# Optimization experiments

Hardware: AMD Instinct MI355X
Metric: run time of the kernel (lower is better)

Reference implementation:

```python
import jax, jax.numpy as jnp
import numpy as np

B, IN, OUT = 2048, 64, 2048


def setup_inputs() -> dict:
    key = jax.random.key(0)
    k1, k2, k3 = jax.random.split(key, 3)
    x = jax.random.normal(k1, (B, IN), dtype=jnp.float32)
    # learned params (shapes per init: means [in, out], inv_std_dev [out, in, in])
    means = jax.random.uniform(k2, (IN, OUT), dtype=jnp.float32)
    # roughly like the inverse of a diagonal step matrix plus small noise
    inv_std_dev = (jax.random.normal(k3, (OUT, IN, IN), dtype=jnp.float32) * 0.05
                   + jnp.eye(IN, dtype=jnp.float32) * 0.5)
    return {"x": x, "means": means, "inv_std_dev": inv_std_dev}


def reference(x, means, inv_std_dev):
    # diff[b, o, i] = x[b, i] - means[i, o]   -> [B, OUT, IN]
    d = x[:, None, :] - means.T[None, :, :]
    # torch uses inv_std_dev.pow(2) (elementwise square), not a matrix square
    A = inv_std_dev * inv_std_dev  # [OUT, IN, IN]
    # per-neuron quadratic form: q[b, o] = d[b,o,:] @ A[o] @ d[b,o,:]
    q = jnp.einsum('boi,oij,boj->bo', d, A, d)
    return jnp.exp(-0.5 * q)  # [B, OUT]
```

## Files before the change

### kernel.cpp

```cpp
#include <hip/hip_runtime.h>
#include <hip/hip_bf16.h>

typedef __bf16 bf16x8 __attribute__((ext_vector_type(8)));
typedef float f32x4 __attribute__((ext_vector_type(4)));
typedef float f32x16 __attribute__((ext_vector_type(16)));

#define B_N 2048
#define O_N 2048
#define K_TRI 2080
#define K_TOT 2304
#define K_STEPS 36
#define STEP_B 131072

__device__ __forceinline__ void gld16(const void* g, void* l) {
    __builtin_amdgcn_global_load_lds(
        (const __attribute__((address_space(1))) void*)g,
        (__attribute__((address_space(3))) void*)l,
        16, 0, 0);
}

__global__ __launch_bounds__(256) void rbf_prepA(
    const float* __restrict__ inv, const float* __restrict__ means,
    const float* __restrict__ x, __bf16* __restrict__ Srm,
    __bf16* __restrict__ Pt)
{
    __shared__ float s[64 * 65];
    __shared__ float mld[64];
    __shared__ float uw[128];
    __shared__ unsigned short ptab[K_TRI];

    const int t = threadIdx.x;
    {
        int base = 0;
#pragma unroll 1
        for (int i = 0; i < 64; ++i) {
            if (t < 64 - i) ptab[base + t] = (unsigned short)((i << 8) | (i + t));
            base += 64 - i;
        }
    }

    if ((int)blockIdx.x < O_N) {
        const int o = blockIdx.x;
        const float4* src = (const float4*)(inv + (size_t)o * 4096);
#pragma unroll
        for (int k = 0; k < 4; ++k) {
            const int idx = k * 256 + t;
            const float4 v = src[idx];
            const int i = idx >> 4;
            const int j0 = (idx & 15) * 4;
            s[i * 65 + j0 + 0] = v.x * v.x;
            s[i * 65 + j0 + 1] = v.y * v.y;
            s[i * 65 + j0 + 2] = v.z * v.z;
            s[i * 65 + j0 + 3] = v.w * v.w;
        }
        if (t < 64) mld[t] = means[(size_t)t * O_N + o];
        __syncthreads();
        if (t < 64) {
            float u = 0.f;
#pragma unroll
            for (int i = 0; i < 64; ++i) u = fmaf(s[i * 65 + t], mld[i], u);
            uw[t] = u;
        } else if (t < 128) {
            const int j = t - 64;
            float w = 0.f;
#pragma unroll
            for (int i = 0; i < 64; ++i) w = fmaf(s[j * 65 + i], mld[i], w);
            uw[64 + j] = w;
        }
        __syncthreads();
        __bf16* Srow = Srm + (size_t)o * K_TOT;
#pragma unroll 1
        for (int c = t; c < K_TOT; c += 256) {
            float v;
            if (c < K_TRI) {
                const int ij = ptab[c];
                const int i = ij >> 8, j = ij & 255;
                v = (i == j) ? s[i * 65 + i] : (s[i * 65 + j] + s[j * 65 + i]);
            } else if (c < 2272) {
                const int j = (c - K_TRI) & 63;
                const float cv = -(uw[j] + uw[64 + j]);
                const __bf16 hi = (__bf16)cv;
                v = (c < 2208) ? (float)hi : (cv - (float)hi);
            } else if (c < 2274) {
                float kk = 0.f;
#pragma unroll
                for (int j = 0; j < 64; ++j) kk = fmaf(uw[j], mld[j], kk);
                const __bf16 khi = (__bf16)kk;
                v = (c == 2272) ? (float)khi : (kk - (float)khi);
            } else v = 0.f;
            Srow[c] = (__bf16)v;
        }
    } else {
        const int b0r = ((int)blockIdx.x - O_N) * 8;
#pragma unroll
        for (int q = 0; q < 2; ++q) {
            const int idx = q * 256 + t;
            s[(idx >> 6) * 65 + (idx & 63)] =
                x[(size_t)(b0r + (idx >> 6)) * 64 + (idx & 63)];
        }
        __syncthreads();
#pragma unroll 1
        for (int q = 0; q < 9; ++q) {
            const int task = q * 256 + t;
            const int c8 = task >> 3, r8 = task & 7;
            const float* xr = &s[r8 * 65];
            unsigned short w8[8];
#pragma unroll
            for (int e = 0; e < 8; ++e) {
                const int c = c8 * 8 + e;
                float v;
                if (c < K_TRI) {
                    const int ij = ptab[c];
                    v = xr[ij >> 8] * xr[ij & 255];
                } else if (c < 2272) {
                    const float xv = xr[(c - K_TRI) & 63];
                    const __bf16 hi = (__bf16)xv;
                    v = (c < 2144) ? (float)hi
                      : (c < 2208) ? (xv - (float)hi) : (float)hi;
                } else if (c < 2274) v = 1.f;
                else v = 0.f;
                w8[e] = __builtin_bit_cast(unsigned short, (__bf16)v);
            }
            *(bf16x8*)(Pt + ((size_t)c8 * 2048 + b0r + r8) * 8) =
                *(const bf16x8*)w8;
        }
    }
}

__global__ __launch_bounds__(256, 2) void rbf_prepB(
    const __bf16* __restrict__ Srm, __bf16* __restrict__ St)
{
    __shared__ __align__(16) char ts[64 * 1156];
    const int t = threadIdx.x;
    const int tb = (int)blockIdx.x >> 2;
    const int cp = (int)blockIdx.x & 3;
    const int o0 = tb * 64;

#pragma unroll 1
    for (int q = 0; q < 18; ++q) {
        const int idx = q * 256 + t;
        const int r = idx / 72, c = idx % 72;
        const float4 v = *(const float4*)((const char*)Srm
                          + (size_t)(o0 + r) * (K_TOT * 2) + cp * 1152 + c * 16);
        *(float4*)(&ts[r * 1156 + c * 16]) = v;
    }
    __syncthreads();
#pragma unroll 1
    for (int q = 0; q < 18; ++q) {
        const int idx = q * 256 + t;
        const int c = idx >> 6, r = idx & 63;
        const float4 v = *(const float4*)(&ts[r * 1156 + c * 16]);
        *(float4*)((char*)St + ((size_t)(cp * 72 + c) * 2048 + o0 + r) * 16) = v;
    }
}

__global__ __launch_bounds__(256, 2) void rbf_gemm_sk(
    const __bf16* __restrict__ P, const __bf16* __restrict__ S,
    float* __restrict__ Cpart)
{
    __shared__ __align__(16) char sAB[4][16384];

    const int tid = threadIdx.x;
    const int lane = tid & 63;
    const int w = tid >> 6;
    const int wr = w >> 1, wc = w & 1;
    const int cl = lane & 31;
    const int h = lane >> 5;

    const int wg = (int)blockIdx.x;
    const int xcd = wg & 7;
    const int loc = wg >> 3;
    const int kh = loc & 1;
    const int opan = (loc >> 1) & 1;
    const int bpan = loc >> 2;
    const int oBase = (xcd * 2 + opan) * 128;
    const int bBase = bpan * 128;
    const int kc = kh * 144;

    const char* gsrc[4];
#pragma unroll
    for (int q = 0; q < 4; ++q) {
        const int ks = (q & 1) * 2 + (tid >> 7);
        const int row = tid & 127;
        gsrc[q] = (q < 2)
            ? (const char*)P + ((size_t)(kc + ks) * 2048 + bBase + row) * 16
            : (const char*)S + ((size_t)(kc + ks) * 2048 + oBase + row) * 16;
    }

#define RBF_STAGE(ST) do {                                                    \
    const size_t go_ = (size_t)(ST) * STEP_B;                                 \
    char* d_ = &sAB[(ST) & 3][0];                                             \
    gld16(gsrc[0] + go_, d_ + 0    + tid * 16);                               \
    gld16(gsrc[1] + go_, d_ + 4096 + tid * 16);                               \
    gld16(gsrc[2] + go_, d_ + 8192  + tid * 16);                              \
    gld16(gsrc[3] + go_, d_ + 12288 + tid * 16);                              \
} while (0)

    RBF_STAGE(0);
    RBF_STAGE(1);

    const f32x16 zz = {0.f,0.f,0.f,0.f,0.f,0.f,0.f,0.f,
                       0.f,0.f,0.f,0.f,0.f,0.f,0.f,0.f};
    f32x16 acc00 = zz, acc01 = zz, acc10 = zz, acc11 = zz;

    const int aoff = (wr * 64 + cl) * 16;
    const int boff = 8192 + (wc * 64 + cl) * 16;

#pragma unroll 1
    for (int st = 0; st < K_STEPS; ++st) {
        if (st + 2 < K_STEPS) {
            RBF_STAGE(st + 2);
            asm volatile("s_waitcnt vmcnt(8)" ::: "memory");
        } else if (st + 1 < K_STEPS) {
            asm volatile("s_waitcnt vmcnt(4)" ::: "memory");
        } else {
            asm volatile("s_waitcnt vmcnt(0)" ::: "memory");
        }
        __builtin_amdgcn_s_barrier();
        __builtin_amdgcn_sched_barrier(0);
        const char* bp = &sAB[st & 3][0];

        __builtin_amdgcn_s_setprio(1);
#pragma unroll
        for (int s = 0; s < 2; ++s) {
            const int kso = (s * 2 + h) * 2048;
            const bf16x8 a0 = *(const bf16x8*)(bp + kso + aoff);
            const bf16x8 a1 = *(const bf16x8*)(bp + kso + aoff + 512);
            const bf16x8 b0 = *(const bf16x8*)(bp + kso + boff);
            const bf16x8 b1 = *(const bf16x8*)(bp + kso + boff + 512);
            acc00 = __builtin_amdgcn_mfma_f32_32x32x16_bf16(a0, b0, acc00, 0, 0, 0);
            acc01 = __builtin_amdgcn_mfma_f32_32x32x16_bf16(a0, b1, acc01, 0, 0, 0);
            acc10 = __builtin_amdgcn_mfma_f32_32x32x16_bf16(a1, b0, acc10, 0, 0, 0);
            acc11 = __builtin_amdgcn_mfma_f32_32x32x16_bf16(a1, b1, acc11, 0, 0, 0);
        }
        __builtin_amdgcn_s_setprio(0);
    }
#undef RBF_STAGE

    float* Cp = Cpart + (size_t)kh * O_N * B_N;
#pragma unroll
    for (int r = 0; r < 16; ++r) {
        const int row32 = (r & 3) + 8 * (r >> 2) + 4 * h;
        const size_t r0 = (size_t)(bBase + wr * 64 + row32) * O_N;
        const size_t r1 = (size_t)(bBase + wr * 64 + 32 + row32) * O_N;
        const int c0 = oBase + wc * 64 + cl;
        const int c1 = oBase + wc * 64 + 32 + cl;
        Cp[r0 + c0] = acc00[r];
        Cp[r0 + c1] = acc01[r];
        Cp[r1 + c0] = acc10[r];
        Cp[r1 + c1] = acc11[r];
    }
}

__global__ __launch_bounds__(256) void rbf_reduce(
    const float* __restrict__ C0, const float* __restrict__ C1,
    float* __restrict__ out)
{
    const size_t base = ((size_t)blockIdx.x * 256 + threadIdx.x) * 8;
#pragma unroll
    for (int q = 0; q < 2; ++q) {
        const size_t i = base + q * 4;
        const f32x4 a = *(const f32x4*)(C0 + i);
        const f32x4 b = *(const f32x4*)(C1 + i);
        f32x4 r;
#pragma unroll
        for (int e = 0; e < 4; ++e)
            r[e] = exp2f((a[e] + b[e]) * -0.72134752044448170368f);
        *(f32x4*)(out + i) = r;
    }
}

extern "C" void kernel_launch(void* const* d_in, const int* in_sizes, int n_in,
                              void* d_out, int out_size, void* d_ws, size_t ws_size,
                              hipStream_t stream)
{
    const float* x = (const float*)d_in[0];
    const float* means = (const float*)d_in[1];
    const float* inv = (const float*)d_in[2];
    float* out = (float*)d_out;

    const size_t SZ = (size_t)O_N * K_TOT * sizeof(__bf16);
    const size_t CZ = (size_t)O_N * B_N * sizeof(float);
    __bf16* St  = (__bf16*)d_ws;
    __bf16* Pt  = (__bf16*)((char*)d_ws + SZ);
    __bf16* Srm = (__bf16*)((char*)d_ws + 2 * SZ);
    float*  C0  = (float*)((char*)d_ws + 3 * SZ);
    float*  C1  = (float*)((char*)d_ws + 3 * SZ + CZ);

    rbf_prepA<<<dim3(O_N + 256), dim3(256), 0, stream>>>(inv, means, x, Srm, Pt);
    rbf_prepB<<<dim3(128), dim3(256), 0, stream>>>(Srm, St);
    rbf_gemm_sk<<<dim3(512), dim3(256), 0, stream>>>(Pt, St, C0);
    rbf_reduce<<<dim3(2048), dim3(256), 0, stream>>>(C0, C1, out);

    (void)in_sizes; (void)n_in; (void)out_size; (void)ws_size;
}
```

Before: 70.02 us.

## Enlarge GEMM block tile to 256x128 with 8 waves and triple-buffered LDS

Each GEMM workgroup grows to 512 threads covering a 256(B) x 128(O) output tile, with 8 K-chunks per step over 18 steps. The 4-deep 16KB LDS ring becomes a 3-deep 48KB ring, and the prefetch is now issued after the barrier. The grid halves to 256 workgroups. The larger tile is meant to cut global-to-LDS traffic per MFMA by reusing the O panel across more rows, but the ~144KB of LDS likely allows only one workgroup per CU and leaves fewer blocks to hide latency.

```diff
diff --git a/kernel.cpp b/kernel.cpp
--- a/kernel.cpp
+++ b/kernel.cpp
@@ -9,8 +9,8 @@
 #define O_N 2048
 #define K_TRI 2080
 #define K_TOT 2304
-#define K_STEPS 36
-#define STEP_B 131072
+#define N_STEPS 18
+#define STEP_B 262144
 
 __device__ __forceinline__ void gld16(const void* g, void* l) {
     __builtin_amdgcn_global_load_lds(
@@ -154,16 +154,17 @@
     }
 }
 
-__global__ __launch_bounds__(256, 2) void rbf_gemm_sk(
+__global__ __launch_bounds__(512, 2) void rbf_gemm_sk(
     const __bf16* __restrict__ P, const __bf16* __restrict__ S,
     float* __restrict__ Cpart)
 {
-    __shared__ __align__(16) char sAB[4][16384];
+    __shared__ __align__(16) char sAB[3][49152];
 
     const int tid = threadIdx.x;
     const int lane = tid & 63;
     const int w = tid >> 6;
-    const int wr = w >> 1, wc = w & 1;
+    const int wr = w >> 1;
+    const int wc = w & 1;
     const int cl = lane & 31;
     const int h = lane >> 5;
 
@@ -171,29 +172,35 @@
     const int xcd = wg & 7;
     const int loc = wg >> 3;
     const int kh = loc & 1;
-    const int opan = (loc >> 1) & 1;
-    const int bpan = loc >> 2;
-    const int oBase = (xcd * 2 + opan) * 128;
-    const int bBase = bpan * 128;
-    const int kc = kh * 144;
-
-    const char* gsrc[4];
-#pragma unroll
-    for (int q = 0; q < 4; ++q) {
-        const int ks = (q & 1) * 2 + (tid >> 7);
-        const int row = tid & 127;
-        gsrc[q] = (q < 2)
-            ? (const char*)P + ((size_t)(kc + ks) * 2048 + bBase + row) * 16
-            : (const char*)S + ((size_t)(kc + ks) * 2048 + oBase + row) * 16;
+    const int rest = loc >> 1;
+    const int opan = xcd * 2 + (rest & 1);
+    const int bpan = rest >> 1;
+    const int oBase = opan * 128;
+    const int bBase = bpan * 256;
+    const int kcb = kh * 144;
+
+    const char* gsrc[6];
+    int ldst[6];
+#pragma unroll
+    for (int r = 0; r < 6; ++r) {
+        if (r < 4) {
+            const int ch = 2 * r + (tid >> 8);
+            const int row = tid & 255;
+            ldst[r] = r * 8192 + tid * 16;
+            gsrc[r] = (const char*)P + ((size_t)(kcb + ch) * 2048 + bBase + row) * 16;
+        } else {
+            const int ch = (r - 4) * 4 + (tid >> 7);
+            const int row = tid & 127;
+            ldst[r] = 32768 + (r - 4) * 8192 + tid * 16;
+            gsrc[r] = (const char*)S + ((size_t)(kcb + ch) * 2048 + oBase + row) * 16;
+        }
     }
 
 #define RBF_STAGE(ST) do {                                                    \
     const size_t go_ = (size_t)(ST) * STEP_B;                                 \
-    char* d_ = &sAB[(ST) & 3][0];                                             \
-    gld16(gsrc[0] + go_, d_ + 0    + tid * 16);                               \
-    gld16(gsrc[1] + go_, d_ + 4096 + tid * 16);                               \
-    gld16(gsrc[2] + go_, d_ + 8192  + tid * 16);                              \
-    gld16(gsrc[3] + go_, d_ + 12288 + tid * 16);                              \
+    char* d_ = &sAB[(ST) % 3][0];                                             \
+    _Pragma("unroll")                                                         \
+    for (int r_ = 0; r_ < 6; ++r_) gld16(gsrc[r_] + go_, d_ + ldst[r_]);      \
 } while (0)
 
     RBF_STAGE(0);
@@ -204,30 +211,29 @@
     f32x16 acc00 = zz, acc01 = zz, acc10 = zz, acc11 = zz;
 
     const int aoff = (wr * 64 + cl) * 16;
-    const int boff = 8192 + (wc * 64 + cl) * 16;
-
-#pragma unroll 1
-    for (int st = 0; st < K_STEPS; ++st) {
-        if (st + 2 < K_STEPS) {
-            RBF_STAGE(st + 2);
-            asm volatile("s_waitcnt vmcnt(8)" ::: "memory");
-        } else if (st + 1 < K_STEPS) {
-            asm volatile("s_waitcnt vmcnt(4)" ::: "memory");
+    const int boff = 32768 + (wc * 64 + cl) * 16;
+
+#pragma unroll 1
+    for (int st = 0; st < N_STEPS; ++st) {
+        if (st < N_STEPS - 1) {
+            asm volatile("s_waitcnt vmcnt(6)" ::: "memory");
         } else {
             asm volatile("s_waitcnt vmcnt(0)" ::: "memory");
         }
         __builtin_amdgcn_s_barrier();
+        if (st + 2 < N_STEPS) RBF_STAGE(st + 2);
         __builtin_amdgcn_sched_barrier(0);
-        const char* bp = &sAB[st & 3][0];
+        const char* bp = &sAB[st % 3][0];
 
         __builtin_amdgcn_s_setprio(1);
 #pragma unroll
-        for (int s = 0; s < 2; ++s) {
-            const int kso = (s * 2 + h) * 2048;
-            const bf16x8 a0 = *(const bf16x8*)(bp + kso + aoff);
-            const bf16x8 a1 = *(const bf16x8*)(bp + kso + aoff + 512);
-            const bf16x8 b0 = *(const bf16x8*)(bp + kso + boff);
-            const bf16x8 b1 = *(const bf16x8*)(bp + kso + boff + 512);
+        for (int ks = 0; ks < 4; ++ks) {
+            const int ca = (2 * ks + h) * 4096 + aoff;
+            const int cb = (2 * ks + h) * 2048 + boff;
+            const bf16x8 a0 = *(const bf16x8*)(bp + ca);
+            const bf16x8 a1 = *(const bf16x8*)(bp + ca + 512);
+            const bf16x8 b0 = *(const bf16x8*)(bp + cb);
+            const bf16x8 b1 = *(const bf16x8*)(bp + cb + 512);
             acc00 = __builtin_amdgcn_mfma_f32_32x32x16_bf16(a0, b0, acc00, 0, 0, 0);
             acc01 = __builtin_amdgcn_mfma_f32_32x32x16_bf16(a0, b1, acc01, 0, 0, 0);
             acc10 = __builtin_amdgcn_mfma_f32_32x32x16_bf16(a1, b0, acc10, 0, 0, 0);
@@ -289,7 +295,7 @@
 
     rbf_prepA<<<dim3(O_N + 256), dim3(256), 0, stream>>>(inv, means, x, Srm, Pt);
     rbf_prepB<<<dim3(128), dim3(256), 0, stream>>>(Srm, St);
-    rbf_gemm_sk<<<dim3(512), dim3(256), 0, stream>>>(Pt, St, C0);
+    rbf_gemm_sk<<<dim3(256), dim3(512), 0, stream>>>(Pt, St, C0);
     rbf_reduce<<<dim3(2048), dim3(256), 0, stream>>>(C0, C1, out);
 
     (void)in_sizes; (void)n_in; (void)out_size; (void)ws_size;
```

Measured after the change: 70.04 us. About the same (+0.0%).
